# Kernel optimization log

Hardware: AMD Instinct MI355X
Metric: run time of the kernel (lower is better)

The kernel has to match this reference:

```python
import jax, jax.numpy as jnp
import numpy as np

D = 3  # input dim, hardcoded in source


def _jet_linear(c0, c1, c2, W, b):
    # Taylor-mode (raw-derivative coefficients) through y = x @ W^T + b.
    # Bias only affects the 0th coefficient; higher coefficients are linear.
    y0 = jnp.einsum('bdi,oi->bdo', c0, W) + b
    y1 = jnp.einsum('bdi,oi->bdo', c1, W)
    y2 = jnp.einsum('bdi,oi->bdo', c2, W)
    return y0, y1, y2


def _jet_tanh(c0, c1, c2):
    # g(t) with g(0)=c0, g'(0)=c1, g''(0)=c2; f = tanh(g):
    #   f(0)  = tanh(c0)
    #   f'(0) = sech^2(c0) * c1
    #   f''(0)= sech^2(c0) * c2 - 2 tanh(c0) sech^2(c0) * c1^2
    y0 = jnp.tanh(c0)
    s = 1.0 - y0 * y0  # sech^2
    y1 = s * c1
    y2 = s * c2 - 2.0 * y0 * s * (c1 * c1)
    return y0, y1, y2


def setup_inputs() -> dict:
    key = jax.random.key(0)
    ks = jax.random.split(key, 7)
    B = 131072
    x = jax.random.normal(ks[0], (B, D), dtype=jnp.float32)
    # Kaiming-ish small init so tanh does not saturate
    W1 = jax.random.normal(ks[1], (128, D), dtype=jnp.float32) * (1.0 / np.sqrt(D))
    b1 = jax.random.normal(ks[2], (128,), dtype=jnp.float32) * 0.01
    W2 = jax.random.normal(ks[3], (64, 128), dtype=jnp.float32) * (1.0 / np.sqrt(128))
    b2 = jax.random.normal(ks[4], (64,), dtype=jnp.float32) * 0.01
    W3 = jax.random.normal(ks[5], (1, 64), dtype=jnp.float32) * (1.0 / np.sqrt(64))
    b3 = jax.random.normal(ks[6], (1,), dtype=jnp.float32) * 0.01
    return {'x': x, 'W1': W1, 'b1': b1, 'W2': W2, 'b2': b2, 'W3': W3, 'b3': b3}


def reference(x, W1, b1, W2, b2, W3, b3):
    # x: [B, D]. Propagate a k=2 jet along each of the D coordinate
    # directions (vmapped over the direction axis d), then sum the 2nd
    # coefficients -> Laplacian. Returns [B, 1].
    B = x.shape[0]
    dt = x.dtype
    X0 = jnp.broadcast_to(x[:, None, :], (B, D, D))            # replicate(x, D)
    X1 = jnp.broadcast_to(jnp.eye(D, dtype=dt), (B, D, D))     # eye(D)
    X2 = jnp.zeros((B, D, D), dtype=dt)                         # zeros(D, D)
    c = _jet_linear(X0, X1, X2, W1, b1)
    c = _jet_tanh(*c)
    c = _jet_linear(*c, W2, b2)
    c = _jet_tanh(*c)
    F0, F1, F2 = _jet_linear(*c, W3, b3)                        # F2: [B, D, 1]
    return F2.sum(axis=1)                                       # sum_vmapped -> [B, 1]
```

## Files before the change

kernel.cpp:

```cpp
#include <hip/hip_runtime.h>


typedef _Float16 h2 __attribute__((ext_vector_type(2)));
typedef _Float16 h4 __attribute__((ext_vector_type(4)));
typedef _Float16 h8 __attribute__((ext_vector_type(8)));
typedef float f32x4 __attribute__((ext_vector_type(4)));

#define BLOCK 256
constexpr int DH1 = 128;
constexpr int DH2 = 64;
constexpr int TILES = 2;
constexpr float CTANH = 2.885390081777926814f;

__device__ __forceinline__ h2 pk(float a, float b) {
    auto r = __builtin_amdgcn_cvt_pkrtz(a, b);
    return __builtin_bit_cast(h2, r);
}

__device__ __forceinline__ float pkf(float a, float b) {
    return __builtin_bit_cast(float, __builtin_amdgcn_cvt_pkrtz(a, b));
}

__device__ __forceinline__ h2 pkmul(h2 a, float bbits) {
    float af = __builtin_bit_cast(float, a);
    float r;
    asm("v_pk_mul_f16 %0, %1, %2" : "=v"(r) : "v"(af), "v"(bbits));
    return __builtin_bit_cast(h2, r);
}

__device__ __forceinline__ h8 cat4(h2 a, h2 b, h2 c, h2 d) {
    h4 lo = __builtin_shufflevector(a, b, 0, 1, 2, 3);
    h4 hi = __builtin_shufflevector(c, d, 0, 1, 2, 3);
    return __builtin_shufflevector(lo, hi, 0, 1, 2, 3, 4, 5, 6, 7);
}

__global__ __launch_bounds__(BLOCK) void lap_fused(
        const float* __restrict__ x,
        const float* __restrict__ W1, const float* __restrict__ b1,
        const float* __restrict__ W2, const float* __restrict__ b2,
        const float* __restrict__ W3,
        float* __restrict__ out, int B, int ntiles)
{
    __shared__ float4 s_w1p[DH1];
    __shared__ f32x4  s_wpk[DH1/2];
    __shared__ __align__(16) _Float16 s_a[16][64][8];
    __shared__ __align__(16) float s_b2c[DH2];
    __shared__ __align__(16) float s_w3[DH2];

    const int t    = threadIdx.x;
    const int lane = t & 63;
    const int wave = t >> 6;
    const int bcol = lane & 15;
    const int g    = lane >> 4;

    float xv[TILES][3];
    #pragma unroll
    for (int tile = 0; tile < TILES; ++tile) {
        const int tid  = blockIdx.x + tile * gridDim.x;
        const int braw = tid * 64 + wave * 16 + bcol;
        const int b    = (braw < B) ? braw : (B - 1);
        xv[tile][0] = x[b*3+0];
        xv[tile][1] = x[b*3+1];
        xv[tile][2] = x[b*3+2];
    }

    #pragma unroll
    for (int u = 0; u < 4; ++u) {
        const int f   = u * 256 + t;
        const int l   = f & 63;
        const int row = f >> 6;
        const int m   = row & 3;
        const int kk  = row >> 2;
        const int k   = m * 16 + (l & 15);
        const int jr  = kk * 32 + (l >> 4) * 8;
        const float4 wlo = *reinterpret_cast<const float4*>(W2 + k * DH1 + jr);
        const float4 whi = *reinterpret_cast<const float4*>(W2 + k * DH1 + jr + 4);
        *reinterpret_cast<h8*>(&s_a[row][l][0]) =
            cat4(pk(wlo.x, wlo.y), pk(wlo.z, wlo.w),
                 pk(whi.x, whi.y), pk(whi.z, whi.w));
    }
    if (t < DH1) {
        const float wx = W1[t*3+0], wy = W1[t*3+1], wz = W1[t*3+2];
        s_w1p[t] = make_float4(wx, wy, wz, CTANH * b1[t]);
    }
    if (t < DH1/2) {
        const float wxe = W1[6*t+0], wye = W1[6*t+1], wze = W1[6*t+2];
        const float wxo = W1[6*t+3], wyo = W1[6*t+4], wzo = W1[6*t+5];
        const float qe  = -2.0f * (wxe*wxe + wye*wye + wze*wze);
        const float qo  = -2.0f * (wxo*wxo + wyo*wyo + wzo*wzo);
        f32x4 v;
        v[0] = pkf(wxe, wxo);
        v[1] = pkf(wye, wyo);
        v[2] = pkf(wze, wzo);
        v[3] = pkf(qe,  qo);
        s_wpk[t] = v;
    }
    if (t < DH2) { s_b2c[t] = CTANH * b2[t]; s_w3[t] = W3[t]; }
    __syncthreads();

    #pragma unroll 1
    for (int tile = 0; tile < TILES; ++tile) {
        const int tid = blockIdx.x + tile * gridDim.x;
        if (tid >= ntiles) break;
        const int braw = tid * 64 + wave * 16 + bcol;

        const float x0c = xv[tile][0] * CTANH;
        const float x1c = xv[tile][1] * CTANH;
        const float x2c = xv[tile][2] * CTANH;

        f32x4 acc[5][4];
        #pragma unroll
        for (int f = 0; f < 5; ++f)
            #pragma unroll
            for (int m = 0; m < 4; ++m)
                acc[f][m] = (f32x4){0.f, 0.f, 0.f, 0.f};

        #pragma unroll
        for (int kk = 0; kk < 4; ++kk) {
            h2 P0[4], P1[4], P2[4], P3[4], P4[4];
            #pragma unroll
            for (int ii = 0; ii < 4; ++ii) {
                const int j0 = kk*32 + g*8 + ii*2;
                const float4 wa = s_w1p[j0];
                const float4 wb = s_w1p[j0 + 1];
                const f32x4  wp = s_wpk[j0 >> 1];

                const float prea = fmaf(x0c, wa.x, fmaf(x1c, wa.y, fmaf(x2c, wa.z, wa.w)));
                const float ea   = __builtin_amdgcn_exp2f(prea);
                const float ra   = __builtin_amdgcn_rcpf(ea + 1.0f);
                const float ha   = fmaf(-2.0f, ra, 1.0f);
                const float sa   = fmaf(-ha, ha, 1.0f);

                const float preb = fmaf(x0c, wb.x, fmaf(x1c, wb.y, fmaf(x2c, wb.z, wb.w)));
                const float eb   = __builtin_amdgcn_exp2f(preb);
                const float rb   = __builtin_amdgcn_rcpf(eb + 1.0f);
                const float hb   = fmaf(-2.0f, rb, 1.0f);
                const float sb   = fmaf(-hb, hb, 1.0f);

                const h2 S  = pk(sa, sb);
                const h2 HS = pk(ha * sa, hb * sb);
                P0[ii] = pk(ha, hb);
                P1[ii] = pkmul(S,  wp[0]);
                P2[ii] = pkmul(S,  wp[1]);
                P3[ii] = pkmul(S,  wp[2]);
                P4[ii] = pkmul(HS, wp[3]);
            }
            const h8 F0 = cat4(P0[0], P0[1], P0[2], P0[3]);
            const h8 F1 = cat4(P1[0], P1[1], P1[2], P1[3]);
            const h8 F2 = cat4(P2[0], P2[1], P2[2], P2[3]);
            const h8 F3 = cat4(P3[0], P3[1], P3[2], P3[3]);
            const h8 F4 = cat4(P4[0], P4[1], P4[2], P4[3]);

            #pragma unroll
            for (int m = 0; m < 4; ++m) {
                const h8 fa = *reinterpret_cast<const h8*>(&s_a[kk*4 + m][lane][0]);
                acc[0][m] = __builtin_amdgcn_mfma_f32_16x16x32_f16(fa, F0, acc[0][m], 0, 0, 0);
                acc[1][m] = __builtin_amdgcn_mfma_f32_16x16x32_f16(fa, F1, acc[1][m], 0, 0, 0);
                acc[2][m] = __builtin_amdgcn_mfma_f32_16x16x32_f16(fa, F2, acc[2][m], 0, 0, 0);
                acc[3][m] = __builtin_amdgcn_mfma_f32_16x16x32_f16(fa, F3, acc[3][m], 0, 0, 0);
                acc[4][m] = __builtin_amdgcn_mfma_f32_16x16x32_f16(fa, F4, acc[4][m], 0, 0, 0);
            }
        }

        float partial = 0.0f;
        #pragma unroll
        for (int m = 0; m < 4; ++m) {
            const int kb = m*16 + g*4;
            const f32x4 b2v = *reinterpret_cast<const f32x4*>(&s_b2c[kb]);
            const f32x4 w3v = *reinterpret_cast<const f32x4*>(&s_w3[kb]);
            #pragma unroll
            for (int r = 0; r < 4; ++r) {
                const float e0 = __builtin_amdgcn_exp2f(fmaf(CTANH, acc[0][m][r], b2v[r]));
                const float g0 = fmaf(-2.0f, __builtin_amdgcn_rcpf(e0 + 1.0f), 1.0f);
                const float s2 = fmaf(-g0, g0, 1.0f);
                const float qd = acc[1][m][r]*acc[1][m][r]
                               + acc[2][m][r]*acc[2][m][r]
                               + acc[3][m][r]*acc[3][m][r];
                const float G2 = s2 * fmaf(-2.0f * g0, qd, acc[4][m][r]);
                partial = fmaf(w3v[r], G2, partial);
            }
        }

        partial += __shfl_xor(partial, 16);
        partial += __shfl_xor(partial, 32);

        if (g == 0 && braw < B) out[braw] = partial;
    }
}

extern "C" void kernel_launch(void* const* d_in, const int* in_sizes, int n_in,
                              void* d_out, int out_size, void* d_ws, size_t ws_size,
                              hipStream_t stream) {
    const float* x  = (const float*)d_in[0];
    const float* W1 = (const float*)d_in[1];
    const float* b1 = (const float*)d_in[2];
    const float* W2 = (const float*)d_in[3];
    const float* b2 = (const float*)d_in[4];
    const float* W3 = (const float*)d_in[5];
    float* out = (float*)d_out;

    const int B      = in_sizes[0] / 3;
    const int ntiles = (B + 63) / 64;
    const int grid   = (ntiles + TILES - 1) / TILES;
    lap_fused<<<grid, BLOCK, 0, stream>>>(x, W1, b1, W2, b2, W3, out, B, ntiles);
}
```

Measured before the change: 24.83 us.

## Compute layer-1 preactivations with MFMA instead of scalar FMAs

```diff
diff --git a/kernel.cpp b/kernel.cpp
--- a/kernel.cpp
+++ b/kernel.cpp
@@ -41,9 +41,9 @@
         const float* __restrict__ W3,
         float* __restrict__ out, int B, int ntiles)
 {
-    __shared__ float4 s_w1p[DH1];
+    __shared__ __align__(16) _Float16 s_a [16][64][8];
+    __shared__ __align__(16) _Float16 s_a1[ 8][64][8];
     __shared__ f32x4  s_wpk[DH1/2];
-    __shared__ __align__(16) _Float16 s_a[16][64][8];
     __shared__ __align__(16) float s_b2c[DH2];
     __shared__ __align__(16) float s_w3[DH2];
 
@@ -72,16 +72,33 @@
         const int m   = row & 3;
         const int kk  = row >> 2;
         const int k   = m * 16 + (l & 15);
-        const int jr  = kk * 32 + (l >> 4) * 8;
-        const float4 wlo = *reinterpret_cast<const float4*>(W2 + k * DH1 + jr);
-        const float4 whi = *reinterpret_cast<const float4*>(W2 + k * DH1 + jr + 4);
+        const int gl  = l >> 4;
+        const int j0  = kk * 32 + gl * 4;
+        const int j1  = kk * 32 + 16 + gl * 4;
+        const float4 w0 = *reinterpret_cast<const float4*>(W2 + k * DH1 + j0);
+        const float4 w1 = *reinterpret_cast<const float4*>(W2 + k * DH1 + j1);
         *reinterpret_cast<h8*>(&s_a[row][l][0]) =
-            cat4(pk(wlo.x, wlo.y), pk(wlo.z, wlo.w),
-                 pk(whi.x, whi.y), pk(whi.z, whi.w));
-    }
-    if (t < DH1) {
-        const float wx = W1[t*3+0], wy = W1[t*3+1], wz = W1[t*3+2];
-        s_w1p[t] = make_float4(wx, wy, wz, CTANH * b1[t]);
+            cat4(pk(w0.x, w0.y), pk(w0.z, w0.w),
+                 pk(w1.x, w1.y), pk(w1.z, w1.w));
+    }
+    {
+        const h2 z2 = pk(0.0f, 0.0f);
+        #pragma unroll
+        for (int v = 0; v < 2; ++v) {
+            const int e  = v * 256 + t;
+            const int m1 = e >> 6;
+            const int l  = e & 63;
+            const int gl = l >> 4;
+            const int jp = m1 * 16 + (l & 15);
+            h8 frag;
+            if (gl == 0) {
+                const float wx = W1[jp*3+0], wy = W1[jp*3+1], wz = W1[jp*3+2];
+                frag = cat4(pk(wx, wy), pk(wz, CTANH * b1[jp]), z2, z2);
+            } else {
+                frag = cat4(z2, z2, z2, z2);
+            }
+            *reinterpret_cast<h8*>(&s_a1[m1][l][0]) = frag;
+        }
     }
     if (t < DH1/2) {
         const float wxe = W1[6*t+0], wye = W1[6*t+1], wze = W1[6*t+2];
@@ -108,6 +125,11 @@
         const float x1c = xv[tile][1] * CTANH;
         const float x2c = xv[tile][2] * CTANH;
 
+        const h2 z2 = pk(0.0f, 0.0f);
+        h2 xlo = z2, xhi = z2;
+        if (g == 0) { xlo = pk(x0c, x1c); xhi = pk(x2c, 1.0f); }
+        const h8 B1 = cat4(xlo, xhi, z2, z2);
+
         f32x4 acc[5][4];
         #pragma unroll
         for (int f = 0; f < 5; ++f)
@@ -119,31 +141,35 @@
         for (int kk = 0; kk < 4; ++kk) {
             h2 P0[4], P1[4], P2[4], P3[4], P4[4];
             #pragma unroll
-            for (int ii = 0; ii < 4; ++ii) {
-                const int j0 = kk*32 + g*8 + ii*2;
-                const float4 wa = s_w1p[j0];
-                const float4 wb = s_w1p[j0 + 1];
-                const f32x4  wp = s_wpk[j0 >> 1];
-
-                const float prea = fmaf(x0c, wa.x, fmaf(x1c, wa.y, fmaf(x2c, wa.z, wa.w)));
-                const float ea   = __builtin_amdgcn_exp2f(prea);
-                const float ra   = __builtin_amdgcn_rcpf(ea + 1.0f);
-                const float ha   = fmaf(-2.0f, ra, 1.0f);
-                const float sa   = fmaf(-ha, ha, 1.0f);
-
-                const float preb = fmaf(x0c, wb.x, fmaf(x1c, wb.y, fmaf(x2c, wb.z, wb.w)));
-                const float eb   = __builtin_amdgcn_exp2f(preb);
-                const float rb   = __builtin_amdgcn_rcpf(eb + 1.0f);
-                const float hb   = fmaf(-2.0f, rb, 1.0f);
-                const float sb   = fmaf(-hb, hb, 1.0f);
-
-                const h2 S  = pk(sa, sb);
-                const h2 HS = pk(ha * sa, hb * sb);
-                P0[ii] = pk(ha, hb);
-                P1[ii] = pkmul(S,  wp[0]);
-                P2[ii] = pkmul(S,  wp[1]);
-                P3[ii] = pkmul(S,  wp[2]);
-                P4[ii] = pkmul(HS, wp[3]);
+            for (int u = 0; u < 2; ++u) {
+                const int m1 = kk*2 + u;
+                const h8 fa1 = *reinterpret_cast<const h8*>(&s_a1[m1][lane][0]);
+                const f32x4 pr = __builtin_amdgcn_mfma_f32_16x16x32_f16(
+                    fa1, B1, (f32x4){0.f, 0.f, 0.f, 0.f}, 0, 0, 0);
+                #pragma unroll
+                for (int v = 0; v < 2; ++v) {
+                    const int pi = u*2 + v;
+                    const f32x4 wp = s_wpk[m1*8 + g*2 + v];
+
+                    const float prea = pr[v*2+0];
+                    const float preb = pr[v*2+1];
+                    const float ea   = __builtin_amdgcn_exp2f(prea);
+                    const float ra   = __builtin_amdgcn_rcpf(ea + 1.0f);
+                    const float ha   = fmaf(-2.0f, ra, 1.0f);
+                    const float sa   = fmaf(-ha, ha, 1.0f);
+                    const float eb   = __builtin_amdgcn_exp2f(preb);
+                    const float rb   = __builtin_amdgcn_rcpf(eb + 1.0f);
+                    const float hb   = fmaf(-2.0f, rb, 1.0f);
+                    const float sb   = fmaf(-hb, hb, 1.0f);
+
+                    const h2 S  = pk(sa, sb);
+                    const h2 HS = pk(ha * sa, hb * sb);
+                    P0[pi] = pk(ha, hb);
+                    P1[pi] = pkmul(S,  wp[0]);
+                    P2[pi] = pkmul(S,  wp[1]);
+                    P3[pi] = pkmul(S,  wp[2]);
+                    P4[pi] = pkmul(HS, wp[3]);
+                }
             }
             const h8 F0 = cat4(P0[0], P0[1], P0[2], P0[3]);
             const h8 F1 = cat4(P1[0], P1[1], P1[2], P1[3]);
```

After: 23.75 us. -4.3%, faster.
